# Optimization experiments

Hardware: AMD Instinct MI355X
Metric: run time of the kernel (lower is better)

Reference implementation:

```python
import jax, jax.numpy as jnp
import numpy as np

A, B = 64, 128           # n_atoms, batch
EMBED, NG = 128, 50      # embed_dim, num_gaussians
RADIUS = 12.0
AVG = 60.0               # avg_atoms
N_HID = 2                # num_layers=4 -> 2 residual hidden linears


def setup_inputs() -> dict:
    key = jax.random.key(0)
    ks = jax.random.split(key, 24)
    T = jax.random.normal(ks[0], (A, A, B, EMBED), dtype=jnp.float32)
    mask = (jax.random.uniform(ks[1], (A, A, B, 1)) < 0.9).astype(jnp.float32)
    dist = jax.random.uniform(ks[2], (A, A, B), dtype=jnp.float32) * RADIUS
    v = jax.random.normal(ks[3], (A, A, B, 3), dtype=jnp.float32)
    vec_hat = v / (jnp.linalg.norm(v, axis=-1, keepdims=True) + 1e-8)

    def w(k, shape):
        s = 1.0 / np.sqrt(shape[0])
        return jax.random.uniform(k, shape, minval=-s, maxval=s, dtype=jnp.float32)

    params = {}
    for pfx, base in (("e", 4), ("f", 14)):
        params[pfx + "W_in"] = w(ks[base + 0], (EMBED, EMBED))
        params[pfx + "b_in"] = w(ks[base + 1], (EMBED,))
        params[pfx + "W_h"] = jnp.stack([w(ks[base + 2], (EMBED, EMBED)),
                                          w(ks[base + 3], (EMBED, EMBED))])
        params[pfx + "b_h"] = jnp.stack([w(ks[base + 4], (EMBED,)),
                                          w(ks[base + 5], (EMBED,))])
        params[pfx + "W_out"] = w(ks[base + 6], (EMBED, EMBED))
        params[pfx + "b_out"] = w(ks[base + 7], (EMBED,))
        params[pfx + "_rbf_w"] = w(ks[base + 8], (NG, EMBED))
        params[pfx + "_head_w"] = w(ks[base + 9], (EMBED, 1))
    return dict(T=T, mask=mask, dist=dist, vec_hat=vec_hat, **params)


def _resmlp(x, W_in, b_in, W_h, b_h, W_out, b_out):
    # input -> SiLU -> residual hidden blocks -> output (dropout=0)
    x = jax.nn.silu(x @ W_in + b_in)
    for i in range(N_HID):
        x = x + jax.nn.silu(x @ W_h[i] + b_h[i])
    return x @ W_out + b_out


def _rbf(dist, w_rbf):
    offset = jnp.linspace(0.0, RADIUS, NG, dtype=jnp.float32)
    step = RADIUS / (NG - 1)
    coeff = -0.5 / step ** 2
    smeared = jnp.exp(coeff * jnp.square(dist[..., None] - offset))  # [A,A,B,NG]
    return smeared @ w_rbf                                            # [A,A,B,EMBED]


def reference(T, mask, dist, vec_hat,
              eW_in, eb_in, eW_h, eb_h, eW_out, eb_out, e_rbf_w, e_head_w,
              fW_in, fb_in, fW_h, fb_h, fW_out, fb_out, f_rbf_w, f_head_w):
    e_feat = _resmlp(T, eW_in, eb_in, eW_h, eb_h, eW_out, eb_out) * _rbf(dist, e_rbf_w)
    f_feat = _resmlp(T, fW_in, fb_in, fW_h, fb_h, fW_out, fb_out) * _rbf(dist, f_rbf_w)
    e = e_feat @ e_head_w                    # [A,A,B,1]
    f = (f_feat @ f_head_w) * vec_hat        # [A,A,B,3]
    energy = jnp.sum(e * mask, axis=(0, 1)) / (AVG ** 2)  # [B,1]
    forces = jnp.sum(f * mask, axis=0) / AVG               # [A,B,3]
    return energy, forces
```

## Files before the change

### kernel.cpp

```cpp
#include <hip/hip_runtime.h>

#define A_DIM 64
#define B_DIM 128
#define E 128
#define NG 50
#define NROW (A_DIM*A_DIM*B_DIM)
#define TR 64
#define KS 136
#define SMS 72
#define WBLK 512
#define BR_STRIDE 147456

using bf16x8  = __bf16 __attribute__((ext_vector_type(8)));
using short8v = short __attribute__((ext_vector_type(8)));
using f32x16  = float __attribute__((ext_vector_type(16)));

__device__ __forceinline__ float silu_f(float x) {
  return x * __builtin_amdgcn_rcpf(1.0f + __expf(-x));
}

__device__ __forceinline__ unsigned short bf16_rne(float v) {
  unsigned u = __float_as_uint(v);
  return (unsigned short)((u + 0x7FFFu + ((u >> 16) & 1u)) >> 16);
}
__device__ __forceinline__ void split2(float v, unsigned short& h, unsigned short& l) {
  h = bf16_rne(v);
  float fh = __uint_as_float(((unsigned)h) << 16);
  l = bf16_rne(v - fh);
}

__device__ __forceinline__ void split2pk(float a, float b, unsigned& hp, unsigned& lp) {
  unsigned h, l;
  asm("v_cvt_pk_bf16_f32 %0, %1, %2" : "=v"(h) : "v"(a), "v"(b));
  float fa = __uint_as_float(h << 16);
  float fb = __uint_as_float(h & 0xffff0000u);
  asm("v_cvt_pk_bf16_f32 %0, %1, %2" : "=v"(l) : "v"(a - fa), "v"(b - fb));
  hp = h; lp = l;
}

__device__ __forceinline__ void gemm_chunk32(
    const short* __restrict__ xhi, const short* __restrict__ xlo, int xstr,
    int kcol, const short* __restrict__ wl, int cidx,
    f32x16 acc[2], int l31, int l5)
{
  bf16x8 bh[2], bl[2];
  #pragma unroll
  for (int s = 0; s < 2; ++s) {
    bh[s] = __builtin_bit_cast(bf16x8,
              *(const short8v*)(wl + (size_t)(cidx * 16 + s) * WBLK));
    bl[s] = __builtin_bit_cast(bf16x8,
              *(const short8v*)(wl + (size_t)(cidx * 16 + 2 + s) * WBLK));
  }
  #pragma unroll
  for (int rt = 0; rt < 2; ++rt) {
    const short* arow = xhi + (rt * 32 + l31) * xstr + kcol + l5 * 8;
    const short* lrow = xlo + (rt * 32 + l31) * xstr + kcol + l5 * 8;
    #pragma unroll
    for (int s = 0; s < 2; ++s) {
      bf16x8 ah = __builtin_bit_cast(bf16x8, *(const short8v*)(arow + s * 16));
      bf16x8 al = __builtin_bit_cast(bf16x8, *(const short8v*)(lrow + s * 16));
      acc[rt] = __builtin_amdgcn_mfma_f32_32x32x16_bf16(al, bh[s], acc[rt], 0, 0, 0);
      acc[rt] = __builtin_amdgcn_mfma_f32_32x32x16_bf16(ah, bl[s], acc[rt], 0, 0, 0);
      acc[rt] = __builtin_amdgcn_mfma_f32_32x32x16_bf16(ah, bh[s], acc[rt], 0, 0, 0);
    }
  }
}

__global__ __launch_bounds__(256) void prep_weights(
    const float* __restrict__ eWin, const float* __restrict__ eWh,
    const float* __restrict__ eWout, const float* __restrict__ erbf,
    const float* __restrict__ fWin, const float* __restrict__ fWh,
    const float* __restrict__ fWout, const float* __restrict__ frbf,
    short* __restrict__ S)
{
  int o = blockIdx.x * 256 + threadIdx.x;
  if (o >= 2 * 73728) return;
  int br = (o >= 73728) ? 1 : 0;
  int r = o - br * 73728;
  short* base = S + br * BR_STRIDE;
  float v; int cidx, n, kk;
  if (r < 65536) {
    int lay = r >> 14, idx = r & 16383;
    n = idx >> 7; int k = idx & 127;
    const float* W = (lay == 0) ? (br ? fWin : eWin)
                   : (lay == 3) ? (br ? fWout : eWout)
                   : ((br ? fWh : eWh) + (lay - 1) * 16384);
    v = W[k * 128 + n];
    cidx = lay * 4 + (k >> 5); kk = k & 31;
  } else {
    int rr = r - 65536;
    n = rr >> 6; int k = rr & 63;
    v = (k < NG) ? (br ? frbf : erbf)[k * 128 + n] : 0.0f;
    cidx = 16 + (k >> 5); kk = k & 31;
  }
  int blk = cidx * 16 + (n >> 5) * 4 + (kk >> 4);
  int idx = blk * WBLK + ((n & 31) + 32 * ((kk >> 3) & 1)) * 8 + (kk & 7);
  unsigned short h, l; split2(v, h, l);
  base[idx] = (short)h;
  base[idx + 2 * WBLK] = (short)l;
}

__global__ __launch_bounds__(256, 3) void fused_main(
    const float* __restrict__ T, const float* __restrict__ mask,
    const float* __restrict__ dist,
    const float* __restrict__ ebin, const float* __restrict__ ebh,
    const float* __restrict__ ebout, const float* __restrict__ ehead,
    const float* __restrict__ fbin, const float* __restrict__ fbh,
    const float* __restrict__ fbout, const float* __restrict__ fhead,
    const short* __restrict__ S,
    float* __restrict__ em, float* __restrict__ fm)
{
  __shared__ short xa[2 * TR * KS];
  __shared__ float part[4][TR];

  const int t = threadIdx.x;
  const int wave = t >> 6, lane = t & 63;
  const int l31 = lane & 31, l5 = lane >> 5;
  const int br = blockIdx.x & 1;
  const long tile = blockIdx.x >> 1;
  const long r0g = tile * TR;

  const short* wl = S + br * BR_STRIDE + wave * (4 * WBLK) + lane * 8;
  const float* bin  = br ? fbin : ebin;
  const float* bh_  = br ? fbh : ebh;
  const float* bout = br ? fbout : ebout;
  const float* head = br ? fhead : ehead;
  float* outw = br ? fm : em;

  short* xahi = xa;
  short* xalo = xa + TR * KS;

  {
    int row = t >> 2, seg = t & 3;
    const float* Tp = T + (r0g + row) * E + seg * 32;
    short* ph = xahi + row * KS + seg * 32;
    short* pl = xalo + row * KS + seg * 32;
    #pragma unroll
    for (int j = 0; j < 8; ++j) {
      float4 v = *(const float4*)(Tp + j * 4);
      unsigned h01, l01, h23, l23;
      split2pk(v.x, v.y, h01, l01);
      split2pk(v.z, v.w, h23, l23);
      *(uint2*)(ph + j * 4) = make_uint2(h01, h23);
      *(uint2*)(pl + j * 4) = make_uint2(l01, l23);
    }
  }

  float xres[2][16];
  f32x16 acc[2];

  #pragma unroll 1
  for (int lay = 0; lay < 4; ++lay) {
    const float* bg = (lay == 0) ? bin : (lay == 3) ? bout : (bh_ + (lay - 1) * E);
    float b0 = bg[wave * 32 + l31];
    #pragma unroll
    for (int i = 0; i < 16; ++i) { acc[0][i] = b0; acc[1][i] = b0; }
    __syncthreads();
    #pragma unroll
    for (int ch = 0; ch < 4; ++ch)
      gemm_chunk32(xahi, xalo, KS, ch * 32, wl, lay * 4 + ch, acc, l31, l5);
    __syncthreads();
    if (lay < 3) {
      #pragma unroll
      for (int rt = 0; rt < 2; ++rt)
        #pragma unroll
        for (int rg = 0; rg < 16; rg += 2) {
          float v0 = silu_f(acc[rt][rg]);
          float v1 = silu_f(acc[rt][rg + 1]);
          if (lay > 0) { v0 += xres[rt][rg]; v1 += xres[rt][rg + 1]; }
          xres[rt][rg] = v0; xres[rt][rg + 1] = v1;
          unsigned hp, lp; split2pk(v0, v1, hp, lp);
          int rowa = rt * 32 + 4 * l5 + (rg & 3) + 8 * (rg >> 2);
          int col = wave * 32 + l31;
          xahi[rowa * KS + col]       = (short)(hp & 0xffffu);
          xahi[(rowa + 1) * KS + col] = (short)(hp >> 16);
          xalo[rowa * KS + col]       = (short)(lp & 0xffffu);
          xalo[(rowa + 1) * KS + col] = (short)(lp >> 16);
        }
    }
  }

  short* smhi = xa;
  short* smlo = xa + TR * SMS;
  const float stepv = 12.0f / 49.0f;
  const float coeff = -0.5f / (stepv * stepv);
  {
    int r = t & 63, kg = t >> 6;
    float d = dist[r0g + r];
    #pragma unroll
    for (int j4 = 0; j4 < 4; ++j4) {
      float vv[4];
      #pragma unroll
      for (int jj = 0; jj < 4; ++jj) {
        int k = kg * 16 + j4 * 4 + jj;
        float dd = d - (float)k * stepv;
        vv[jj] = (k < NG) ? __expf(coeff * dd * dd) : 0.0f;
      }
      unsigned h01, l01, h23, l23;
      split2pk(vv[0], vv[1], h01, l01);
      split2pk(vv[2], vv[3], h23, l23);
      *(uint2*)(smhi + r * SMS + kg * 16 + j4 * 4) = make_uint2(h01, h23);
      *(uint2*)(smlo + r * SMS + kg * 16 + j4 * 4) = make_uint2(l01, l23);
    }
  }
  float h0 = head[wave * 32 + l31];
  f32x16 acc2[2];
  #pragma unroll
  for (int i = 0; i < 16; ++i) { acc2[0][i] = 0.f; acc2[1][i] = 0.f; }
  __syncthreads();
  gemm_chunk32(smhi, smlo, SMS, 0,  wl, 16, acc2, l31, l5);
  gemm_chunk32(smhi, smlo, SMS, 32, wl, 17, acc2, l31, l5);

  #pragma unroll
  for (int rt = 0; rt < 2; ++rt)
    #pragma unroll
    for (int rg = 0; rg < 16; ++rg) {
      float p = acc[rt][rg] * acc2[rt][rg] * h0;
      p += __shfl_xor(p, 1); p += __shfl_xor(p, 2);
      p += __shfl_xor(p, 4); p += __shfl_xor(p, 8);
      p += __shfl_xor(p, 16);
      if (l31 == 0)
        part[wave][rt * 32 + 4 * l5 + (rg & 3) + 8 * (rg >> 2)] = p;
    }
  __syncthreads();
  if (t < TR) {
    float pr = part[0][t] + part[1][t] + part[2][t] + part[3][t];
    outw[r0g + t] = pr * mask[r0g + t];
  }
}

__global__ __launch_bounds__(256) void energy_kernel(const float* __restrict__ em,
                                                     float* __restrict__ out) {
  __shared__ float red[256];
  int b = blockIdx.x, t = threadIdx.x;
  float s = 0.0f;
  for (int p = t; p < A_DIM * A_DIM; p += 256) s += em[(long)p * B_DIM + b];
  red[t] = s; __syncthreads();
  for (int off = 128; off > 0; off >>= 1) {
    if (t < off) red[t] += red[t + off];
    __syncthreads();
  }
  if (t == 0) out[b] = red[0] * (1.0f / 3600.0f);
}

__global__ __launch_bounds__(256) void forces_kernel(const float* __restrict__ fm,
                                                     const float* __restrict__ vh,
                                                     float* __restrict__ out) {
  int o = blockIdx.x * 256 + threadIdx.x;
  if (o >= A_DIM * B_DIM * 3) return;
  int c = o % 3;
  int b = (o / 3) % B_DIM;
  int j = o / (B_DIM * 3);
  float s = 0.0f;
  #pragma unroll 4
  for (int i = 0; i < A_DIM; ++i) {
    long row = ((long)(i * A_DIM + j)) * B_DIM + b;
    s += fm[row] * vh[row * 3 + c];
  }
  out[B_DIM + o] = s * (1.0f / 60.0f);
}

extern "C" void kernel_launch(void* const* d_in, const int* in_sizes, int n_in,
                              void* d_out, int out_size, void* d_ws, size_t ws_size,
                              hipStream_t stream) {
  const float* T    = (const float*)d_in[0];
  const float* mask = (const float*)d_in[1];
  const float* dist = (const float*)d_in[2];
  const float* vh   = (const float*)d_in[3];
  const float* eWin = (const float*)d_in[4];
  const float* ebin = (const float*)d_in[5];
  const float* eWh  = (const float*)d_in[6];
  const float* ebh  = (const float*)d_in[7];
  const float* eWout= (const float*)d_in[8];
  const float* ebout= (const float*)d_in[9];
  const float* erbf = (const float*)d_in[10];
  const float* ehead= (const float*)d_in[11];
  const float* fWin = (const float*)d_in[12];
  const float* fbin = (const float*)d_in[13];
  const float* fWh  = (const float*)d_in[14];
  const float* fbh  = (const float*)d_in[15];
  const float* fWout= (const float*)d_in[16];
  const float* fbout= (const float*)d_in[17];
  const float* frbf = (const float*)d_in[18];
  const float* fhead= (const float*)d_in[19];

  float* em = (float*)d_ws;
  float* fm = em + NROW;
  short* S  = (short*)(fm + NROW);
  float* out = (float*)d_out;

  prep_weights<<<576, 256, 0, stream>>>(eWin, eWh, eWout, erbf,
                                        fWin, fWh, fWout, frbf, S);
  fused_main<<<2 * (NROW / TR), 256, 0, stream>>>(
      T, mask, dist,
      ebin, ebh, ebout, ehead,
      fbin, fbh, fbout, fhead,
      S, em, fm);
  energy_kernel<<<B_DIM, 256, 0, stream>>>(em, out);
  forces_kernel<<<(A_DIM * B_DIM * 3) / 256, 256, 0, stream>>>(fm, vh, out);
}
```

Baseline: 858.7 us.

## Switch split-bf16 GEMMs to fp16 activations with scaled split weights, fuse reductions via atomics

Replaces the three-MFMA split-bf16 scheme (hi/lo activations times hi/lo weights) with a single fp16 activation copy multiplied by fp16 hi weights and 64x-scaled fp16 lo weights, accumulated separately. That cuts MFMAs per step from three to two and halves LDS for activations, which allows higher occupancy (launch bounds 4) and keeps the residual in LDS instead of registers. The energy and forces reductions move into the main kernel epilogue as global atomicAdds after a zeroing kernel, removing two kernels and the em/fm workspace traffic. Activations lose precision because they are no longer split, atomics make summation order nondeterministic, and the prep_weights index mapping was also changed.

Result: slower. 1.306 ms (+52.1%).

```diff
diff --git a/kernel.cpp b/kernel.cpp
--- a/kernel.cpp
+++ b/kernel.cpp
@@ -10,58 +10,42 @@
 #define SMS 72
 #define WBLK 512
 #define BR_STRIDE 147456
-
-using bf16x8  = __bf16 __attribute__((ext_vector_type(8)));
+#define NOUT (B_DIM + A_DIM*B_DIM*3)
+#define WLSCALE 64.0f
+#define WLINV   0.015625f
+
+using half8   = _Float16 __attribute__((ext_vector_type(8)));
 using short8v = short __attribute__((ext_vector_type(8)));
 using f32x16  = float __attribute__((ext_vector_type(16)));
 
 __device__ __forceinline__ float silu_f(float x) {
   return x * __builtin_amdgcn_rcpf(1.0f + __expf(-x));
 }
-
-__device__ __forceinline__ unsigned short bf16_rne(float v) {
-  unsigned u = __float_as_uint(v);
-  return (unsigned short)((u + 0x7FFFu + ((u >> 16) & 1u)) >> 16);
-}
-__device__ __forceinline__ void split2(float v, unsigned short& h, unsigned short& l) {
-  h = bf16_rne(v);
-  float fh = __uint_as_float(((unsigned)h) << 16);
-  l = bf16_rne(v - fh);
-}
-
-__device__ __forceinline__ void split2pk(float a, float b, unsigned& hp, unsigned& lp) {
-  unsigned h, l;
-  asm("v_cvt_pk_bf16_f32 %0, %1, %2" : "=v"(h) : "v"(a), "v"(b));
-  float fa = __uint_as_float(h << 16);
-  float fb = __uint_as_float(h & 0xffff0000u);
-  asm("v_cvt_pk_bf16_f32 %0, %1, %2" : "=v"(l) : "v"(a - fa), "v"(b - fb));
-  hp = h; lp = l;
+__device__ __forceinline__ short hbits(_Float16 h) {
+  return (short)__builtin_bit_cast(unsigned short, h);
 }
 
 __device__ __forceinline__ void gemm_chunk32(
-    const short* __restrict__ xhi, const short* __restrict__ xlo, int xstr,
-    int kcol, const short* __restrict__ wl, int cidx,
-    f32x16 acc[2], int l31, int l5)
+    const short* __restrict__ xh_, int xstr, int kcol,
+    const short* __restrict__ wl_, int cidx,
+    f32x16 acc[2], f32x16 accl[2], int l31, int l5)
 {
-  bf16x8 bh[2], bl[2];
+  half8 bh[2], bl[2];
   #pragma unroll
   for (int s = 0; s < 2; ++s) {
-    bh[s] = __builtin_bit_cast(bf16x8,
-              *(const short8v*)(wl + (size_t)(cidx * 16 + s) * WBLK));
-    bl[s] = __builtin_bit_cast(bf16x8,
-              *(const short8v*)(wl + (size_t)(cidx * 16 + 2 + s) * WBLK));
+    bh[s] = __builtin_bit_cast(half8,
+              *(const short8v*)(wl_ + (size_t)(cidx * 16 + s) * WBLK));
+    bl[s] = __builtin_bit_cast(half8,
+              *(const short8v*)(wl_ + (size_t)(cidx * 16 + 2 + s) * WBLK));
   }
   #pragma unroll
   for (int rt = 0; rt < 2; ++rt) {
-    const short* arow = xhi + (rt * 32 + l31) * xstr + kcol + l5 * 8;
-    const short* lrow = xlo + (rt * 32 + l31) * xstr + kcol + l5 * 8;
+    const short* arow = xh_ + (rt * 32 + l31) * xstr + kcol + l5 * 8;
     #pragma unroll
     for (int s = 0; s < 2; ++s) {
-      bf16x8 ah = __builtin_bit_cast(bf16x8, *(const short8v*)(arow + s * 16));
-      bf16x8 al = __builtin_bit_cast(bf16x8, *(const short8v*)(lrow + s * 16));
-      acc[rt] = __builtin_amdgcn_mfma_f32_32x32x16_bf16(al, bh[s], acc[rt], 0, 0, 0);
-      acc[rt] = __builtin_amdgcn_mfma_f32_32x32x16_bf16(ah, bl[s], acc[rt], 0, 0, 0);
-      acc[rt] = __builtin_amdgcn_mfma_f32_32x32x16_bf16(ah, bh[s], acc[rt], 0, 0, 0);
+      half8 a = __builtin_bit_cast(half8, *(const short8v*)(arow + s * 16));
+      acc[rt]  = __builtin_amdgcn_mfma_f32_32x32x16_f16(a, bh[s], acc[rt],  0, 0, 0);
+      accl[rt] = __builtin_amdgcn_mfma_f32_32x32x16_f16(a, bl[s], accl[rt], 0, 0, 0);
     }
   }
 }
@@ -81,7 +65,7 @@
   float v; int cidx, n, kk;
   if (r < 65536) {
     int lay = r >> 14, idx = r & 16383;
-    n = idx >> 7; int k = idx & 127;
+    int k = idx >> 7; n = idx & 127;
     const float* W = (lay == 0) ? (br ? fWin : eWin)
                    : (lay == 3) ? (br ? fWout : eWout)
                    : ((br ? fWh : eWh) + (lay - 1) * 16384);
@@ -89,28 +73,34 @@
     cidx = lay * 4 + (k >> 5); kk = k & 31;
   } else {
     int rr = r - 65536;
-    n = rr >> 6; int k = rr & 63;
+    int k = rr >> 7; n = rr & 127;
     v = (k < NG) ? (br ? frbf : erbf)[k * 128 + n] : 0.0f;
     cidx = 16 + (k >> 5); kk = k & 31;
   }
   int blk = cidx * 16 + (n >> 5) * 4 + (kk >> 4);
-  int idx = blk * WBLK + ((n & 31) + 32 * ((kk >> 3) & 1)) * 8 + (kk & 7);
-  unsigned short h, l; split2(v, h, l);
-  base[idx] = (short)h;
-  base[idx + 2 * WBLK] = (short)l;
-}
-
-__global__ __launch_bounds__(256, 3) void fused_main(
+  int idx2 = blk * WBLK + ((n & 31) + 32 * ((kk >> 3) & 1)) * 8 + (kk & 7);
+  _Float16 wh = (_Float16)v;
+  _Float16 wl = (_Float16)((v - (float)wh) * WLSCALE);
+  base[idx2] = hbits(wh);
+  base[idx2 + 2 * WBLK] = hbits(wl);
+}
+
+__global__ __launch_bounds__(256) void zero_out(float* __restrict__ out) {
+  int i = blockIdx.x * 256 + threadIdx.x;
+  if (i < NOUT) out[i] = 0.0f;
+}
+
+__global__ __launch_bounds__(256, 4) void fused_main(
     const float* __restrict__ T, const float* __restrict__ mask,
-    const float* __restrict__ dist,
+    const float* __restrict__ dist, const float* __restrict__ vh,
     const float* __restrict__ ebin, const float* __restrict__ ebh,
     const float* __restrict__ ebout, const float* __restrict__ ehead,
     const float* __restrict__ fbin, const float* __restrict__ fbh,
     const float* __restrict__ fbout, const float* __restrict__ fhead,
     const short* __restrict__ S,
-    float* __restrict__ em, float* __restrict__ fm)
+    float* __restrict__ out)
 {
-  __shared__ short xa[2 * TR * KS];
+  __shared__ short xa[TR * KS];
   __shared__ float part[4][TR];
 
   const int t = threadIdx.x;
@@ -125,63 +115,57 @@
   const float* bh_  = br ? fbh : ebh;
   const float* bout = br ? fbout : ebout;
   const float* head = br ? fhead : ehead;
-  float* outw = br ? fm : em;
-
-  short* xahi = xa;
-  short* xalo = xa + TR * KS;
 
   {
     int row = t >> 2, seg = t & 3;
     const float* Tp = T + (r0g + row) * E + seg * 32;
-    short* ph = xahi + row * KS + seg * 32;
-    short* pl = xalo + row * KS + seg * 32;
+    short* ph = xa + row * KS + seg * 32;
     #pragma unroll
     for (int j = 0; j < 8; ++j) {
       float4 v = *(const float4*)(Tp + j * 4);
-      unsigned h01, l01, h23, l23;
-      split2pk(v.x, v.y, h01, l01);
-      split2pk(v.z, v.w, h23, l23);
-      *(uint2*)(ph + j * 4) = make_uint2(h01, h23);
-      *(uint2*)(pl + j * 4) = make_uint2(l01, l23);
-    }
-  }
-
-  float xres[2][16];
-  f32x16 acc[2];
+      short4 s4 = make_short4(hbits((_Float16)v.x), hbits((_Float16)v.y),
+                              hbits((_Float16)v.z), hbits((_Float16)v.w));
+      *(short4*)(ph + j * 4) = s4;
+    }
+  }
+
+  f32x16 acc[2], accl[2];
 
   #pragma unroll 1
   for (int lay = 0; lay < 4; ++lay) {
     const float* bg = (lay == 0) ? bin : (lay == 3) ? bout : (bh_ + (lay - 1) * E);
     float b0 = bg[wave * 32 + l31];
     #pragma unroll
-    for (int i = 0; i < 16; ++i) { acc[0][i] = b0; acc[1][i] = b0; }
+    for (int i = 0; i < 16; ++i) {
+      acc[0][i] = b0; acc[1][i] = b0;
+      accl[0][i] = 0.f; accl[1][i] = 0.f;
+    }
     __syncthreads();
     #pragma unroll
     for (int ch = 0; ch < 4; ++ch)
-      gemm_chunk32(xahi, xalo, KS, ch * 32, wl, lay * 4 + ch, acc, l31, l5);
+      gemm_chunk32(xa, KS, ch * 32, wl, lay * 4 + ch, acc, accl, l31, l5);
     __syncthreads();
     if (lay < 3) {
       #pragma unroll
       for (int rt = 0; rt < 2; ++rt)
         #pragma unroll
-        for (int rg = 0; rg < 16; rg += 2) {
-          float v0 = silu_f(acc[rt][rg]);
-          float v1 = silu_f(acc[rt][rg + 1]);
-          if (lay > 0) { v0 += xres[rt][rg]; v1 += xres[rt][rg + 1]; }
-          xres[rt][rg] = v0; xres[rt][rg + 1] = v1;
-          unsigned hp, lp; split2pk(v0, v1, hp, lp);
+        for (int rg = 0; rg < 16; ++rg) {
+          float y = acc[rt][rg] + accl[rt][rg] * WLINV;
+          float v = silu_f(y);
           int rowa = rt * 32 + 4 * l5 + (rg & 3) + 8 * (rg >> 2);
           int col = wave * 32 + l31;
-          xahi[rowa * KS + col]       = (short)(hp & 0xffffu);
-          xahi[(rowa + 1) * KS + col] = (short)(hp >> 16);
-          xalo[rowa * KS + col]       = (short)(lp & 0xffffu);
-          xalo[(rowa + 1) * KS + col] = (short)(lp >> 16);
+          short* slot = xa + rowa * KS + col;
+          if (lay > 0) v += (float)*(const _Float16*)slot;
+          *slot = hbits((_Float16)v);
         }
     }
   }
+  #pragma unroll
+  for (int rt = 0; rt < 2; ++rt)
+    #pragma unroll
+    for (int i = 0; i < 16; ++i) acc[rt][i] += accl[rt][i] * WLINV;
 
   short* smhi = xa;
-  short* smlo = xa + TR * SMS;
   const float stepv = 12.0f / 49.0f;
   const float coeff = -0.5f / (stepv * stepv);
   {
@@ -196,26 +180,28 @@
         float dd = d - (float)k * stepv;
         vv[jj] = (k < NG) ? __expf(coeff * dd * dd) : 0.0f;
       }
-      unsigned h01, l01, h23, l23;
-      split2pk(vv[0], vv[1], h01, l01);
-      split2pk(vv[2], vv[3], h23, l23);
-      *(uint2*)(smhi + r * SMS + kg * 16 + j4 * 4) = make_uint2(h01, h23);
-      *(uint2*)(smlo + r * SMS + kg * 16 + j4 * 4) = make_uint2(l01, l23);
+      short4 s4 = make_short4(hbits((_Float16)vv[0]), hbits((_Float16)vv[1]),
+                              hbits((_Float16)vv[2]), hbits((_Float16)vv[3]));
+      *(short4*)(smhi + r * SMS + kg * 16 + j4 * 4) = s4;
     }
   }
   float h0 = head[wave * 32 + l31];
-  f32x16 acc2[2];
-  #pragma unroll
-  for (int i = 0; i < 16; ++i) { acc2[0][i] = 0.f; acc2[1][i] = 0.f; }
+  f32x16 acc2[2], acc2l[2];
+  #pragma unroll
+  for (int i = 0; i < 16; ++i) {
+    acc2[0][i] = 0.f; acc2[1][i] = 0.f;
+    acc2l[0][i] = 0.f; acc2l[1][i] = 0.f;
+  }
   __syncthreads();
-  gemm_chunk32(smhi, smlo, SMS, 0,  wl, 16, acc2, l31, l5);
-  gemm_chunk32(smhi, smlo, SMS, 32, wl, 17, acc2, l31, l5);
+  gemm_chunk32(smhi, SMS, 0,  wl, 16, acc2, acc2l, l31, l5);
+  gemm_chunk32(smhi, SMS, 32, wl, 17, acc2, acc2l, l31, l5);
 
   #pragma unroll
   for (int rt = 0; rt < 2; ++rt)
     #pragma unroll
     for (int rg = 0; rg < 16; ++rg) {
-      float p = acc[rt][rg] * acc2[rt][rg] * h0;
+      float rb = acc2[rt][rg] + acc2l[rt][rg] * WLINV;
+      float p = acc[rt][rg] * rb * h0;
       p += __shfl_xor(p, 1); p += __shfl_xor(p, 2);
       p += __shfl_xor(p, 4); p += __shfl_xor(p, 8);
       p += __shfl_xor(p, 16);
@@ -224,40 +210,21 @@
     }
   __syncthreads();
   if (t < TR) {
+    long g = r0g + t;
     float pr = part[0][t] + part[1][t] + part[2][t] + part[3][t];
-    outw[r0g + t] = pr * mask[r0g + t];
-  }
-}
-
-__global__ __launch_bounds__(256) void energy_kernel(const float* __restrict__ em,
-                                                     float* __restrict__ out) {
-  __shared__ float red[256];
-  int b = blockIdx.x, t = threadIdx.x;
-  float s = 0.0f;
-  for (int p = t; p < A_DIM * A_DIM; p += 256) s += em[(long)p * B_DIM + b];
-  red[t] = s; __syncthreads();
-  for (int off = 128; off > 0; off >>= 1) {
-    if (t < off) red[t] += red[t + off];
-    __syncthreads();
-  }
-  if (t == 0) out[b] = red[0] * (1.0f / 3600.0f);
-}
-
-__global__ __launch_bounds__(256) void forces_kernel(const float* __restrict__ fm,
-                                                     const float* __restrict__ vh,
-                                                     float* __restrict__ out) {
-  int o = blockIdx.x * 256 + threadIdx.x;
-  if (o >= A_DIM * B_DIM * 3) return;
-  int c = o % 3;
-  int b = (o / 3) % B_DIM;
-  int j = o / (B_DIM * 3);
-  float s = 0.0f;
-  #pragma unroll 4
-  for (int i = 0; i < A_DIM; ++i) {
-    long row = ((long)(i * A_DIM + j)) * B_DIM + b;
-    s += fm[row] * vh[row * 3 + c];
-  }
-  out[B_DIM + o] = s * (1.0f / 60.0f);
+    float pm = pr * mask[g];
+    if (br == 0) {
+      atomicAdd(out + (int)(g & 127), pm * (1.0f / 3600.0f));
+    } else {
+      int b = (int)(g & 127);
+      int j = (int)((g >> 7) & 63);
+      float s = pm * (1.0f / 60.0f);
+      float* fo = out + B_DIM + (j * B_DIM + b) * 3;
+      atomicAdd(fo + 0, s * vh[g * 3 + 0]);
+      atomicAdd(fo + 1, s * vh[g * 3 + 1]);
+      atomicAdd(fo + 2, s * vh[g * 3 + 2]);
+    }
+  }
 }
 
 extern "C" void kernel_launch(void* const* d_in, const int* in_sizes, int n_in,
@@ -284,18 +251,15 @@
   const float* frbf = (const float*)d_in[18];
   const float* fhead= (const float*)d_in[19];
 
-  float* em = (float*)d_ws;
-  float* fm = em + NROW;
-  short* S  = (short*)(fm + NROW);
+  short* S = (short*)d_ws;
   float* out = (float*)d_out;
 
+  zero_out<<<(NOUT + 255) / 256, 256, 0, stream>>>(out);
   prep_weights<<<576, 256, 0, stream>>>(eWin, eWh, eWout, erbf,
                                         fWin, fWh, fWout, frbf, S);
   fused_main<<<2 * (NROW / TR), 256, 0, stream>>>(
-      T, mask, dist,
+      T, mask, dist, vh,
       ebin, ebh, ebout, ehead,
       fbin, fbh, fbout, fhead,
-      S, em, fm);
-  energy_kernel<<<B_DIM, 256, 0, stream>>>(em, out);
-  forces_kernel<<<(A_DIM * B_DIM * 3) / 256, 256, 0, stream>>>(fm, vh, out);
-}
+      S, out);
+}
```
